# Optimization experiments

Hardware: AMD Instinct MI355X
Metric: run time of the kernel (lower is better)

Reference implementation:

```python
import jax, jax.numpy as jnp
import numpy as np

SIZES = [384, 160, 128, 96, 1]   # aev_length followed by hidden sizes (ANI-1 config)
N_SPECIES = 4                    # H, C, N, O
N_LAYERS = 4
CELU_ALPHA = 0.1
B, A = 128, 512                  # molecules, atoms per molecule


def setup_inputs() -> dict:
    key = jax.random.key(0)
    ks = jax.random.split(key, 2 + 2 * N_LAYERS)
    inp = {
        "fullaev": jax.random.normal(ks[0], (B, A, SIZES[0]), dtype=jnp.float32),
        "species": jax.random.randint(ks[1], (A,), 0, N_SPECIES, dtype=jnp.int32),
    }
    # Per-species stacked Linear params, torch default init: U(-1/sqrt(fan_in), 1/sqrt(fan_in))
    for l in range(N_LAYERS):
        bound = 1.0 / np.sqrt(SIZES[l])
        inp[f"W{l}"] = jax.random.uniform(ks[2 + 2 * l], (N_SPECIES, SIZES[l + 1], SIZES[l]),
                                          dtype=jnp.float32, minval=-bound, maxval=bound)
        inp[f"b{l}"] = jax.random.uniform(ks[3 + 2 * l], (N_SPECIES, SIZES[l + 1]),
                                          dtype=jnp.float32, minval=-bound, maxval=bound)
    return inp


def reference(fullaev, species, W0, b0, W1, b1, W2, b2, W3, b3):
    # fullaev: [B, A, aev_len]; species: [A] int route ids.
    # Equivalent to the per-atom Python loop: each atom goes through its
    # species' MLP; gather the per-atom weight matrices and do one batched GEMM per layer.
    Ws = (W0, W1, W2, W3)
    bs = (b0, b1, b2, b3)
    y = fullaev
    for l in range(N_LAYERS):
        Wa = Ws[l][species]          # [A, out, in] gathered per atom
        ba = bs[l][species]          # [A, out]
        y = jnp.einsum('bai,aoi->bao', y, Wa) + ba[None, :, :]
        if l < N_LAYERS - 1:
            y = jax.nn.celu(y, alpha=CELU_ALPHA)
    # stack over atoms + sum reducer over atom dim, then squeeze -> [B]
    return jnp.squeeze(jnp.sum(y, axis=1), axis=-1)
```

## Files before the change

kernel.cpp:

```cpp
#include <hip/hip_runtime.h>
#include <hip/hip_bf16.h>


typedef float f32x4 __attribute__((ext_vector_type(4)));
typedef short s16x8 __attribute__((ext_vector_type(8)));

#define NMOL   128
#define NATOM  512
#define AEV    384
#define MT     64
#define Y0LD   168
#define Y1LD   136
#define Y2LD   104

#define PL0    61440
#define PL1    20480
#define PL2    12288
#define BASE0  0
#define BASE1  245760
#define BASE2  327680
#define WP_BYTE_OFF 262144

typedef const __attribute__((address_space(1))) void* gas_ptr;
typedef __attribute__((address_space(3))) void* las_ptr;

__device__ __forceinline__ ushort f2bf(float f) {
    uint u = __float_as_uint(f);
    return (ushort)((u + 0x7fffu + ((u >> 16) & 1u)) >> 16);
}
__device__ __forceinline__ float bf2f(ushort h) {
    return __uint_as_float(((uint)h) << 16);
}
__device__ __forceinline__ float celu_f(float v) {
    return fmaxf(v, 0.0f) + fminf(0.1f * (__expf(10.0f * v) - 1.0f), 0.0f);
}
__device__ __forceinline__ uint pk2bf(float x, float y) {
    __hip_bfloat162 h2;
    h2.x = __float2bfloat16(x);
    h2.y = __float2bfloat16(y);
    return *(uint*)&h2;
}

__global__ __launch_bounds__(256) void prep_kernel(
    const float* __restrict__ W0, const float* __restrict__ W1,
    const float* __restrict__ W2, ushort* __restrict__ Wp)
{
    const int idx = blockIdx.x * 256 + threadIdx.x;
    int n, k0, KS;
    size_t base;
    const float* src;
    if (idx < 30720) {
        const int s = idx / 7680, r = idx % 7680;
        n = r / 48; k0 = (r % 48) * 8; KS = 12;
        src = W0 + (size_t)idx * 8;
        base = BASE0 + (size_t)s * PL0;
    } else if (idx < 40960) {
        const int i2 = idx - 30720;
        const int s = i2 / 2560, r = i2 % 2560;
        n = r / 20; k0 = (r % 20) * 8; KS = 5;
        src = W1 + (size_t)i2 * 8;
        base = BASE1 + (size_t)s * PL1;
    } else {
        const int i2 = idx - 40960;
        const int s = i2 / 1536, r = i2 % 1536;
        n = r / 16; k0 = (r % 16) * 8; KS = 4;
        src = W2 + (size_t)i2 * 8;
        base = BASE2 + (size_t)s * PL2;
    }
    const float4 v0 = *(const float4*)(src);
    const float4 v1 = *(const float4*)(src + 4);
    const size_t fo = (size_t)((((n >> 4) * KS + (k0 >> 5)) * 64
                                + ((k0 & 31) >> 3) * 16 + (n & 15)) * 8);
    uint4 w;
    w.x = (uint)f2bf(v0.x) | ((uint)f2bf(v0.y) << 16);
    w.y = (uint)f2bf(v0.z) | ((uint)f2bf(v0.w) << 16);
    w.z = (uint)f2bf(v1.x) | ((uint)f2bf(v1.y) << 16);
    w.w = (uint)f2bf(v1.z) | ((uint)f2bf(v1.w) << 16);
    *(uint4*)(Wp + base + fo) = w;
}

__global__ __attribute__((amdgpu_flat_work_group_size(512, 512),
                          amdgpu_waves_per_eu(6, 6)))
void ani_mfma_kernel(
    const float* __restrict__ aev, const int* __restrict__ species,
    const ushort* __restrict__ Wp,
    const float* __restrict__ b0, const float* __restrict__ b1,
    const float* __restrict__ b2,
    const float* __restrict__ W3, const float* __restrict__ b3,
    float* __restrict__ partial)
{
    __shared__ __align__(16) unsigned char smemA[24576];
    __shared__ __align__(16) unsigned char smemB[21504];

    const int bid  = blockIdx.x;
    const int a    = bid >> 1;
    const int half = bid & 1;
    const int tid  = threadIdx.x;
    const int lane = tid & 63;
    const int wid  = tid >> 6;
    const int mgrp = wid >> 2;
    const int ngrp = wid & 3;
    const bool has3 = (ngrp < 2);

    const int s = species[a];
    const ushort* Bh0 = Wp + BASE0 + (size_t)s * PL0;
    const ushort* Bh1 = Wp + BASE1 + (size_t)s * PL1;
    const ushort* Bh2 = Wp + BASE2 + (size_t)s * PL2;
    const float* b0s = b0 + s * 160;
    const float* b1s = b1 + s * 128;
    const float* b2s = b2 + s * 96;
    const float* w3s = W3 + s * 96;
    const float  bb3 = b3[s];

    ushort* y0buf = (ushort*)smemB;
    ushort* y1buf = (ushort*)smemA;

    const int mol8 = lane >> 3;
    const int swz  = (lane & 7) ^ mol8;
    const char* gsrc = (const char*)(aev
        + ((size_t)(half * MT + wid * 8 + mol8) * NATOM + a) * AEV) + swz * 16;
    const int ldsbase = wid * 1024;

    const f32x4 zero = {0.f, 0.f, 0.f, 0.f};
    f32x4 acc[2][3];
    #pragma unroll
    for (int mf = 0; mf < 2; ++mf)
        #pragma unroll
        for (int ti = 0; ti < 3; ++ti) acc[mf][ti] = zero;

    {
        const int r0 = mgrp * 32 + (lane & 15);
        const int c  = lane >> 4;

        __builtin_amdgcn_global_load_lds((gas_ptr)(gsrc),
                                         (las_ptr)(smemA + ldsbase), 16, 0, 0);
        __builtin_amdgcn_global_load_lds((gas_ptr)(gsrc + 128),
                                         (las_ptr)(smemA + 8192 + ldsbase), 16, 0, 0);
        asm volatile("s_waitcnt vmcnt(1)" ::: "memory");
        __builtin_amdgcn_sched_barrier(0);
        __builtin_amdgcn_s_barrier();
        __builtin_amdgcn_sched_barrier(0);

        #pragma unroll
        for (int t = 0; t < 12; ++t) {
            const s16x8 bh0 = *(const s16x8*)(
                Bh0 + ((size_t)((ngrp    ) * 12 + t) * 64 + lane) * 8);
            const s16x8 bh1 = *(const s16x8*)(
                Bh0 + ((size_t)((ngrp + 4) * 12 + t) * 64 + lane) * 8);
            s16x8 bh2;
            if (has3) bh2 = *(const s16x8*)(
                Bh0 + ((size_t)((ngrp + 8) * 12 + t) * 64 + lane) * 8);

            if (t + 2 < 12)
                __builtin_amdgcn_global_load_lds(
                    (gas_ptr)(gsrc + (t + 2) * 128),
                    (las_ptr)(smemA + ((t + 2) % 3) * 8192 + ldsbase), 16, 0, 0);

            const float* Xb = (const float*)(smemA + (t % 3) * 8192);
            s16x8 ah[2];
            #pragma unroll
            for (int mf = 0; mf < 2; ++mf) {
                const int r = r0 + mf * 16;
                const float* rowp = Xb + r * 32;
                const f32x4 c0 = *(const f32x4*)(rowp + (((2 * c    ) ^ (r & 7)) * 4));
                const f32x4 c1 = *(const f32x4*)(rowp + (((2 * c + 1) ^ (r & 7)) * 4));
                union { s16x8 v; uint u[4]; } rr;
                rr.u[0] = pk2bf(c0.x, c0.y);
                rr.u[1] = pk2bf(c0.z, c0.w);
                rr.u[2] = pk2bf(c1.x, c1.y);
                rr.u[3] = pk2bf(c1.z, c1.w);
                ah[mf] = rr.v;
            }
            acc[0][0] = __builtin_amdgcn_mfma_f32_16x16x32_bf16(ah[0], bh0, acc[0][0], 0, 0, 0);
            acc[1][0] = __builtin_amdgcn_mfma_f32_16x16x32_bf16(ah[1], bh0, acc[1][0], 0, 0, 0);
            acc[0][1] = __builtin_amdgcn_mfma_f32_16x16x32_bf16(ah[0], bh1, acc[0][1], 0, 0, 0);
            acc[1][1] = __builtin_amdgcn_mfma_f32_16x16x32_bf16(ah[1], bh1, acc[1][1], 0, 0, 0);
            if (has3) {
                acc[0][2] = __builtin_amdgcn_mfma_f32_16x16x32_bf16(ah[0], bh2, acc[0][2], 0, 0, 0);
                acc[1][2] = __builtin_amdgcn_mfma_f32_16x16x32_bf16(ah[1], bh2, acc[1][2], 0, 0, 0);
            }
            if (t < 11) {
                __builtin_amdgcn_sched_barrier(0);
                __builtin_amdgcn_s_barrier();
                __builtin_amdgcn_sched_barrier(0);
            }
        }
    }

    s16x8 b1r[2][5];
    #pragma unroll
    for (int ks = 0; ks < 5; ++ks) {
        b1r[0][ks] = *(const s16x8*)(Bh1 + ((size_t)((ngrp    ) * 5 + ks) * 64 + lane) * 8);
        b1r[1][ks] = *(const s16x8*)(Bh1 + ((size_t)((ngrp + 4) * 5 + ks) * 64 + lane) * 8);
    }

    #pragma unroll
    for (int ti = 0; ti < 3; ++ti) {
        if (ti < 2 || has3) {
            const int n = (ngrp + 4 * ti) * 16 + (lane & 15);
            const float bv = b0s[n];
            #pragma unroll
            for (int mf = 0; mf < 2; ++mf) {
                #pragma unroll
                for (int r = 0; r < 4; ++r) {
                    const int row = mgrp * 32 + mf * 16 + (lane >> 4) * 4 + r;
                    y0buf[row * Y0LD + n] = f2bf(celu_f(acc[mf][ti][r] + bv));
                }
            }
        }
    }
    __syncthreads();

    f32x4 acc1[2][2];
    #pragma unroll
    for (int mf = 0; mf < 2; ++mf) { acc1[mf][0] = zero; acc1[mf][1] = zero; }
    #pragma unroll
    for (int ks = 0; ks < 5; ++ks) {
        s16x8 ah[2];
        #pragma unroll
        for (int mf = 0; mf < 2; ++mf)
            ah[mf] = *(const s16x8*)(y0buf + (mgrp * 32 + mf * 16 + (lane & 15)) * Y0LD
                                     + ks * 32 + (lane >> 4) * 8);
        #pragma unroll
        for (int mf = 0; mf < 2; ++mf) {
            acc1[mf][0] = __builtin_amdgcn_mfma_f32_16x16x32_bf16(ah[mf], b1r[0][ks], acc1[mf][0], 0, 0, 0);
            acc1[mf][1] = __builtin_amdgcn_mfma_f32_16x16x32_bf16(ah[mf], b1r[1][ks], acc1[mf][1], 0, 0, 0);
        }
    }

    s16x8 b2r[2][4];
    #pragma unroll
    for (int ks = 0; ks < 4; ++ks)
        b2r[0][ks] = *(const s16x8*)(Bh2 + ((size_t)((ngrp) * 4 + ks) * 64 + lane) * 8);
    if (has3) {
        #pragma unroll
        for (int ks = 0; ks < 4; ++ks)
            b2r[1][ks] = *(const s16x8*)(Bh2 + ((size_t)((ngrp + 4) * 4 + ks) * 64 + lane) * 8);
    }

    ushort* Y1 = y1buf;
    #pragma unroll
    for (int t = 0; t < 2; ++t) {
        const int n = (ngrp + 4 * t) * 16 + (lane & 15);
        const float bv = b1s[n];
        #pragma unroll
        for (int mf = 0; mf < 2; ++mf) {
            #pragma unroll
            for (int r = 0; r < 4; ++r) {
                const int row = mgrp * 32 + mf * 16 + (lane >> 4) * 4 + r;
                Y1[row * Y1LD + n] = f2bf(celu_f(acc1[mf][t][r] + bv));
            }
        }
    }
    __syncthreads();

    f32x4 acc2[2][2];
    #pragma unroll
    for (int mf = 0; mf < 2; ++mf) { acc2[mf][0] = zero; acc2[mf][1] = zero; }
    #pragma unroll
    for (int ks = 0; ks < 4; ++ks) {
        s16x8 ah[2];
        #pragma unroll
        for (int mf = 0; mf < 2; ++mf)
            ah[mf] = *(const s16x8*)(Y1 + (mgrp * 32 + mf * 16 + (lane & 15)) * Y1LD
                                     + ks * 32 + (lane >> 4) * 8);
        #pragma unroll
        for (int mf = 0; mf < 2; ++mf) {
            acc2[mf][0] = __builtin_amdgcn_mfma_f32_16x16x32_bf16(ah[mf], b2r[0][ks], acc2[mf][0], 0, 0, 0);
            if (has3)
                acc2[mf][1] = __builtin_amdgcn_mfma_f32_16x16x32_bf16(ah[mf], b2r[1][ks], acc2[mf][1], 0, 0, 0);
        }
    }
    __syncthreads();

    #pragma unroll
    for (int t = 0; t < 2; ++t) {
        if (t == 0 || has3) {
            const int n = (ngrp + 4 * t) * 16 + (lane & 15);
            const float bv = b2s[n];
            #pragma unroll
            for (int mf = 0; mf < 2; ++mf) {
                #pragma unroll
                for (int r = 0; r < 4; ++r) {
                    const int row = mgrp * 32 + mf * 16 + (lane >> 4) * 4 + r;
                    y0buf[row * Y2LD + n] = f2bf(celu_f(acc2[mf][t][r] + bv));
                }
            }
        }
    }
    __syncthreads();

    {
        float* red = (float*)smemA;
        const int m = tid & (MT - 1);
        const int q = tid >> 6;
        float accv = 0.f;
        #pragma unroll
        for (int ii = 0; ii < 12; ++ii) {
            const int i = q * 12 + ii;
            accv = fmaf(w3s[i], bf2f(y0buf[m * Y2LD + i]), accv);
        }
        red[q * MT + m] = accv;
        __syncthreads();
        if (tid < MT) {
            float sm = bb3;
            #pragma unroll
            for (int qq = 0; qq < 8; ++qq) sm += red[qq * MT + tid];
            partial[(size_t)a * NMOL + half * MT + tid] = sm;
        }
    }
}

__global__ __launch_bounds__(256) void reduce_kernel(
    const float* __restrict__ partial, float* __restrict__ out)
{
    __shared__ float red[256];
    const int m = blockIdx.x;
    const int t = threadIdx.x;
    float sv = partial[(size_t)t * NMOL + m] + partial[(size_t)(t + 256) * NMOL + m];
    red[t] = sv;
    __syncthreads();
    #pragma unroll
    for (int w = 128; w > 0; w >>= 1) {
        if (t < w) red[t] += red[t + w];
        __syncthreads();
    }
    if (t == 0) out[m] = red[0];
}

extern "C" void kernel_launch(void* const* d_in, const int* in_sizes, int n_in,
                              void* d_out, int out_size, void* d_ws, size_t ws_size,
                              hipStream_t stream) {
    const float* aev     = (const float*)d_in[0];
    const int*   species = (const int*)  d_in[1];
    const float* W0 = (const float*)d_in[2];
    const float* b0 = (const float*)d_in[3];
    const float* W1 = (const float*)d_in[4];
    const float* b1 = (const float*)d_in[5];
    const float* W2 = (const float*)d_in[6];
    const float* b2 = (const float*)d_in[7];
    const float* W3 = (const float*)d_in[8];
    const float* b3 = (const float*)d_in[9];
    float* out     = (float*)d_out;
    float* partial = (float*)d_ws;
    ushort* Wp     = (ushort*)((char*)d_ws + WP_BYTE_OFF);

    prep_kernel<<<184, 256, 0, stream>>>(W0, W1, W2, Wp);
    ani_mfma_kernel<<<NATOM * 2, 512, 0, stream>>>(aev, species, Wp,
                                                   b0, b1, b2, W3, b3, partial);
    reduce_kernel<<<NMOL, 256, 0, stream>>>(partial, out);
}
```

Before: 46.90 us.

## Stage whole AEV tile as bf16 in LDS upfront instead of pipelined fp32 streaming

Replaces the triple-buffered global_load_lds fp32 pipeline with one bulk load of the 64x384 AEV tile, converted to bf16 once and stored in a single padded LDS buffer. The layer-0 GEMM then runs without per-step barriers. Weight fragments for layers 1 and 2 now load inside the k-loops instead of being prefetched into registers, and one LDS array is reused across all layers. This cuts barriers and repeated conversions but loses the overlap of global loads with MFMA work, and it puts weight loads on the critical path.

```diff
diff --git a/kernel.cpp b/kernel.cpp
--- a/kernel.cpp
+++ b/kernel.cpp
@@ -9,9 +9,13 @@
 #define NATOM  512
 #define AEV    384
 #define MT     64
+#define XLD    392
 #define Y0LD   168
 #define Y1LD   136
 #define Y2LD   104
+
+#define Y1_OFF 10752
+#define RED_OFF 19456
 
 #define PL0    61440
 #define PL1    20480
@@ -20,9 +24,6 @@
 #define BASE1  245760
 #define BASE2  327680
 #define WP_BYTE_OFF 262144
-
-typedef const __attribute__((address_space(1))) void* gas_ptr;
-typedef __attribute__((address_space(3))) void* las_ptr;
 
 __device__ __forceinline__ ushort f2bf(float f) {
     uint u = __float_as_uint(f);
@@ -72,10 +73,10 @@
     const size_t fo = (size_t)((((n >> 4) * KS + (k0 >> 5)) * 64
                                 + ((k0 & 31) >> 3) * 16 + (n & 15)) * 8);
     uint4 w;
-    w.x = (uint)f2bf(v0.x) | ((uint)f2bf(v0.y) << 16);
-    w.y = (uint)f2bf(v0.z) | ((uint)f2bf(v0.w) << 16);
-    w.z = (uint)f2bf(v1.x) | ((uint)f2bf(v1.y) << 16);
-    w.w = (uint)f2bf(v1.z) | ((uint)f2bf(v1.w) << 16);
+    w.x = pk2bf(v0.x, v0.y);
+    w.y = pk2bf(v0.z, v0.w);
+    w.z = pk2bf(v1.x, v1.y);
+    w.w = pk2bf(v1.z, v1.w);
     *(uint4*)(Wp + base + fo) = w;
 }
 
@@ -89,8 +90,7 @@
     const float* __restrict__ W3, const float* __restrict__ b3,
     float* __restrict__ partial)
 {
-    __shared__ __align__(16) unsigned char smemA[24576];
-    __shared__ __align__(16) unsigned char smemB[21504];
+    __shared__ __align__(16) ushort smem[MT * XLD];
 
     const int bid  = blockIdx.x;
     const int a    = bid >> 1;
@@ -112,87 +112,66 @@
     const float* w3s = W3 + s * 96;
     const float  bb3 = b3[s];
 
-    ushort* y0buf = (ushort*)smemB;
-    ushort* y1buf = (ushort*)smemA;
-
-    const int mol8 = lane >> 3;
-    const int swz  = (lane & 7) ^ mol8;
-    const char* gsrc = (const char*)(aev
-        + ((size_t)(half * MT + wid * 8 + mol8) * NATOM + a) * AEV) + swz * 16;
-    const int ldsbase = wid * 1024;
+    ushort* X     = smem;
+    ushort* y0buf = smem;
+    ushort* y1buf = smem + Y1_OFF;
+    ushort* y2buf = smem;
 
     const f32x4 zero = {0.f, 0.f, 0.f, 0.f};
+
+    {
+        const int srow = tid >> 3;
+        const int scol = tid & 7;
+        const float* sp = aev + ((size_t)(half * MT + srow) * NATOM + a) * AEV
+                          + scol * 8;
+        float4 rv[12];
+        #pragma unroll
+        for (int jp = 0; jp < 6; ++jp) {
+            rv[2 * jp]     = *(const float4*)(sp + jp * 64);
+            rv[2 * jp + 1] = *(const float4*)(sp + jp * 64 + 4);
+        }
+        ushort* xd = X + srow * XLD + scol * 8;
+        #pragma unroll
+        for (int jp = 0; jp < 6; ++jp) {
+            uint4 w;
+            w.x = pk2bf(rv[2 * jp].x,     rv[2 * jp].y);
+            w.y = pk2bf(rv[2 * jp].z,     rv[2 * jp].w);
+            w.z = pk2bf(rv[2 * jp + 1].x, rv[2 * jp + 1].y);
+            w.w = pk2bf(rv[2 * jp + 1].z, rv[2 * jp + 1].w);
+            *(uint4*)(xd + jp * 64) = w;
+        }
+    }
+    __syncthreads();
+
     f32x4 acc[2][3];
     #pragma unroll
     for (int mf = 0; mf < 2; ++mf)
         #pragma unroll
         for (int ti = 0; ti < 3; ++ti) acc[mf][ti] = zero;
-
-    {
-        const int r0 = mgrp * 32 + (lane & 15);
-        const int c  = lane >> 4;
-
-        __builtin_amdgcn_global_load_lds((gas_ptr)(gsrc),
-                                         (las_ptr)(smemA + ldsbase), 16, 0, 0);
-        __builtin_amdgcn_global_load_lds((gas_ptr)(gsrc + 128),
-                                         (las_ptr)(smemA + 8192 + ldsbase), 16, 0, 0);
-        asm volatile("s_waitcnt vmcnt(1)" ::: "memory");
-        __builtin_amdgcn_sched_barrier(0);
-        __builtin_amdgcn_s_barrier();
-        __builtin_amdgcn_sched_barrier(0);
-
-        #pragma unroll
-        for (int t = 0; t < 12; ++t) {
+    {
+        const ushort* arow0 = X + (mgrp * 32 + (lane & 15)) * XLD + (lane >> 4) * 8;
+        #pragma unroll
+        for (int gks = 0; gks < 12; ++gks) {
+            s16x8 ah[2];
+            ah[0] = *(const s16x8*)(arow0 + gks * 32);
+            ah[1] = *(const s16x8*)(arow0 + 16 * XLD + gks * 32);
             const s16x8 bh0 = *(const s16x8*)(
-                Bh0 + ((size_t)((ngrp    ) * 12 + t) * 64 + lane) * 8);
+                Bh0 + ((size_t)((ngrp    ) * 12 + gks) * 64 + lane) * 8);
             const s16x8 bh1 = *(const s16x8*)(
-                Bh0 + ((size_t)((ngrp + 4) * 12 + t) * 64 + lane) * 8);
-            s16x8 bh2;
-            if (has3) bh2 = *(const s16x8*)(
-                Bh0 + ((size_t)((ngrp + 8) * 12 + t) * 64 + lane) * 8);
-
-            if (t + 2 < 12)
-                __builtin_amdgcn_global_load_lds(
-                    (gas_ptr)(gsrc + (t + 2) * 128),
-                    (las_ptr)(smemA + ((t + 2) % 3) * 8192 + ldsbase), 16, 0, 0);
-
-            const float* Xb = (const float*)(smemA + (t % 3) * 8192);
-            s16x8 ah[2];
-            #pragma unroll
-            for (int mf = 0; mf < 2; ++mf) {
-                const int r = r0 + mf * 16;
-                const float* rowp = Xb + r * 32;
-                const f32x4 c0 = *(const f32x4*)(rowp + (((2 * c    ) ^ (r & 7)) * 4));
-                const f32x4 c1 = *(const f32x4*)(rowp + (((2 * c + 1) ^ (r & 7)) * 4));
-                union { s16x8 v; uint u[4]; } rr;
-                rr.u[0] = pk2bf(c0.x, c0.y);
-                rr.u[1] = pk2bf(c0.z, c0.w);
-                rr.u[2] = pk2bf(c1.x, c1.y);
-                rr.u[3] = pk2bf(c1.z, c1.w);
-                ah[mf] = rr.v;
-            }
+                Bh0 + ((size_t)((ngrp + 4) * 12 + gks) * 64 + lane) * 8);
             acc[0][0] = __builtin_amdgcn_mfma_f32_16x16x32_bf16(ah[0], bh0, acc[0][0], 0, 0, 0);
             acc[1][0] = __builtin_amdgcn_mfma_f32_16x16x32_bf16(ah[1], bh0, acc[1][0], 0, 0, 0);
             acc[0][1] = __builtin_amdgcn_mfma_f32_16x16x32_bf16(ah[0], bh1, acc[0][1], 0, 0, 0);
             acc[1][1] = __builtin_amdgcn_mfma_f32_16x16x32_bf16(ah[1], bh1, acc[1][1], 0, 0, 0);
             if (has3) {
+                const s16x8 bh2 = *(const s16x8*)(
+                    Bh0 + ((size_t)((ngrp + 8) * 12 + gks) * 64 + lane) * 8);
                 acc[0][2] = __builtin_amdgcn_mfma_f32_16x16x32_bf16(ah[0], bh2, acc[0][2], 0, 0, 0);
                 acc[1][2] = __builtin_amdgcn_mfma_f32_16x16x32_bf16(ah[1], bh2, acc[1][2], 0, 0, 0);
             }
-            if (t < 11) {
-                __builtin_amdgcn_sched_barrier(0);
-                __builtin_amdgcn_s_barrier();
-                __builtin_amdgcn_sched_barrier(0);
-            }
-        }
-    }
-
-    s16x8 b1r[2][5];
-    #pragma unroll
-    for (int ks = 0; ks < 5; ++ks) {
-        b1r[0][ks] = *(const s16x8*)(Bh1 + ((size_t)((ngrp    ) * 5 + ks) * 64 + lane) * 8);
-        b1r[1][ks] = *(const s16x8*)(Bh1 + ((size_t)((ngrp + 4) * 5 + ks) * 64 + lane) * 8);
-    }
+        }
+    }
+    __syncthreads();
 
     #pragma unroll
     for (int ti = 0; ti < 3; ++ti) {
@@ -214,31 +193,24 @@
     f32x4 acc1[2][2];
     #pragma unroll
     for (int mf = 0; mf < 2; ++mf) { acc1[mf][0] = zero; acc1[mf][1] = zero; }
-    #pragma unroll
-    for (int ks = 0; ks < 5; ++ks) {
-        s16x8 ah[2];
-        #pragma unroll
-        for (int mf = 0; mf < 2; ++mf)
-            ah[mf] = *(const s16x8*)(y0buf + (mgrp * 32 + mf * 16 + (lane & 15)) * Y0LD
-                                     + ks * 32 + (lane >> 4) * 8);
-        #pragma unroll
-        for (int mf = 0; mf < 2; ++mf) {
-            acc1[mf][0] = __builtin_amdgcn_mfma_f32_16x16x32_bf16(ah[mf], b1r[0][ks], acc1[mf][0], 0, 0, 0);
-            acc1[mf][1] = __builtin_amdgcn_mfma_f32_16x16x32_bf16(ah[mf], b1r[1][ks], acc1[mf][1], 0, 0, 0);
-        }
-    }
-
-    s16x8 b2r[2][4];
-    #pragma unroll
-    for (int ks = 0; ks < 4; ++ks)
-        b2r[0][ks] = *(const s16x8*)(Bh2 + ((size_t)((ngrp) * 4 + ks) * 64 + lane) * 8);
-    if (has3) {
-        #pragma unroll
-        for (int ks = 0; ks < 4; ++ks)
-            b2r[1][ks] = *(const s16x8*)(Bh2 + ((size_t)((ngrp + 4) * 4 + ks) * 64 + lane) * 8);
-    }
-
-    ushort* Y1 = y1buf;
+    {
+        const ushort* arow0 = y0buf + (mgrp * 32 + (lane & 15)) * Y0LD + (lane >> 4) * 8;
+        #pragma unroll
+        for (int ks = 0; ks < 5; ++ks) {
+            s16x8 ah[2];
+            ah[0] = *(const s16x8*)(arow0 + ks * 32);
+            ah[1] = *(const s16x8*)(arow0 + 16 * Y0LD + ks * 32);
+            const s16x8 bh0 = *(const s16x8*)(
+                Bh1 + ((size_t)((ngrp    ) * 5 + ks) * 64 + lane) * 8);
+            const s16x8 bh1 = *(const s16x8*)(
+                Bh1 + ((size_t)((ngrp + 4) * 5 + ks) * 64 + lane) * 8);
+            acc1[0][0] = __builtin_amdgcn_mfma_f32_16x16x32_bf16(ah[0], bh0, acc1[0][0], 0, 0, 0);
+            acc1[1][0] = __builtin_amdgcn_mfma_f32_16x16x32_bf16(ah[1], bh0, acc1[1][0], 0, 0, 0);
+            acc1[0][1] = __builtin_amdgcn_mfma_f32_16x16x32_bf16(ah[0], bh1, acc1[0][1], 0, 0, 0);
+            acc1[1][1] = __builtin_amdgcn_mfma_f32_16x16x32_bf16(ah[1], bh1, acc1[1][1], 0, 0, 0);
+        }
+    }
+
     #pragma unroll
     for (int t = 0; t < 2; ++t) {
         const int n = (ngrp + 4 * t) * 16 + (lane & 15);
@@ -248,7 +220,7 @@
             #pragma unroll
             for (int r = 0; r < 4; ++r) {
                 const int row = mgrp * 32 + mf * 16 + (lane >> 4) * 4 + r;
-                Y1[row * Y1LD + n] = f2bf(celu_f(acc1[mf][t][r] + bv));
+                y1buf[row * Y1LD + n] = f2bf(celu_f(acc1[mf][t][r] + bv));
             }
         }
     }
@@ -257,21 +229,25 @@
     f32x4 acc2[2][2];
     #pragma unroll
     for (int mf = 0; mf < 2; ++mf) { acc2[mf][0] = zero; acc2[mf][1] = zero; }
-    #pragma unroll
-    for (int ks = 0; ks < 4; ++ks) {
-        s16x8 ah[2];
-        #pragma unroll
-        for (int mf = 0; mf < 2; ++mf)
-            ah[mf] = *(const s16x8*)(Y1 + (mgrp * 32 + mf * 16 + (lane & 15)) * Y1LD
-                                     + ks * 32 + (lane >> 4) * 8);
-        #pragma unroll
-        for (int mf = 0; mf < 2; ++mf) {
-            acc2[mf][0] = __builtin_amdgcn_mfma_f32_16x16x32_bf16(ah[mf], b2r[0][ks], acc2[mf][0], 0, 0, 0);
-            if (has3)
-                acc2[mf][1] = __builtin_amdgcn_mfma_f32_16x16x32_bf16(ah[mf], b2r[1][ks], acc2[mf][1], 0, 0, 0);
-        }
-    }
-    __syncthreads();
+    {
+        const ushort* arow0 = y1buf + (mgrp * 32 + (lane & 15)) * Y1LD + (lane >> 4) * 8;
+        #pragma unroll
+        for (int ks = 0; ks < 4; ++ks) {
+            s16x8 ah[2];
+            ah[0] = *(const s16x8*)(arow0 + ks * 32);
+            ah[1] = *(const s16x8*)(arow0 + 16 * Y1LD + ks * 32);
+            const s16x8 bh0 = *(const s16x8*)(
+                Bh2 + ((size_t)((ngrp) * 4 + ks) * 64 + lane) * 8);
+            acc2[0][0] = __builtin_amdgcn_mfma_f32_16x16x32_bf16(ah[0], bh0, acc2[0][0], 0, 0, 0);
+            acc2[1][0] = __builtin_amdgcn_mfma_f32_16x16x32_bf16(ah[1], bh0, acc2[1][0], 0, 0, 0);
+            if (has3) {
+                const s16x8 bh1 = *(const s16x8*)(
+                    Bh2 + ((size_t)((ngrp + 4) * 4 + ks) * 64 + lane) * 8);
+                acc2[0][1] = __builtin_amdgcn_mfma_f32_16x16x32_bf16(ah[0], bh1, acc2[0][1], 0, 0, 0);
+                acc2[1][1] = __builtin_amdgcn_mfma_f32_16x16x32_bf16(ah[1], bh1, acc2[1][1], 0, 0, 0);
+            }
+        }
+    }
 
     #pragma unroll
     for (int t = 0; t < 2; ++t) {
@@ -283,7 +259,7 @@
                 #pragma unroll
                 for (int r = 0; r < 4; ++r) {
                     const int row = mgrp * 32 + mf * 16 + (lane >> 4) * 4 + r;
-                    y0buf[row * Y2LD + n] = f2bf(celu_f(acc2[mf][t][r] + bv));
+                    y2buf[row * Y2LD + n] = f2bf(celu_f(acc2[mf][t][r] + bv));
                 }
             }
         }
@@ -291,14 +267,14 @@
     __syncthreads();
 
     {
-        float* red = (float*)smemA;
+        float* red = (float*)(smem + RED_OFF);
         const int m = tid & (MT - 1);
         const int q = tid >> 6;
         float accv = 0.f;
         #pragma unroll
         for (int ii = 0; ii < 12; ++ii) {
             const int i = q * 12 + ii;
-            accv = fmaf(w3s[i], bf2f(y0buf[m * Y2LD + i]), accv);
+            accv = fmaf(w3s[i], bf2f(y2buf[m * Y2LD + i]), accv);
         }
         red[q * MT + m] = accv;
         __syncthreads();
```

After: 52.68 us. +12.3%, slower.
